# Performance work log

Measured on AMD Instinct MI355X. Metric: run time of the kernel, lower is better.

## Reference

```python
import jax, jax.numpy as jnp
import numpy as np

B, T, D = 32, 1024, 384
MAX_LEN = 8192

def setup_inputs() -> dict:
    key = jax.random.key(0)
    k1, k2 = jax.random.split(key)
    x = jax.random.normal(k1, (B, T, D), dtype=jnp.float32)
    duration = jax.random.randint(k2, (B, T), 0, 8, dtype=jnp.int32)
    return {"x": x, "duration": duration, "max_len": MAX_LEN}

def reference(x, duration, max_len):
    # x: [B, T, D] float, duration: [B, T] int, max_len: python int
    # Token t occupies output frames [cumsum[t-1], cumsum[t]).
    csum = jnp.cumsum(duration, axis=-1)            # [B, T]
    frames = jnp.arange(max_len, dtype=csum.dtype)  # [L]
    # For frame j, token index = # of cumsum entries <= j (searchsorted right).
    idx = jax.vmap(lambda c: jnp.searchsorted(c, frames, side='right'))(csum)  # [B, L]
    mel_len = csum[:, -1]                           # [B]
    valid = frames[None, :] < mel_len[:, None]      # [B, L]
    idx_c = jnp.clip(idx, 0, x.shape[1] - 1)
    out = jnp.take_along_axis(x, idx_c[:, :, None], axis=1)  # [B, L, D]
    out = jnp.where(valid[:, :, None], out, jnp.zeros((), dtype=x.dtype))
    return out, mel_len.astype(jnp.int32)
```

## Files before the change

kernel.cpp:

```cpp
#include <hip/hip_runtime.h>
#include <hip/hip_bf16.h>


#define LR_B 32
#define LR_T 1024
#define LR_D 384
#define LR_MAXLEN 8192
#define LR_D4 (LR_D / 4)
#define LR_N4 (LR_B * LR_MAXLEN * LR_D4)

__global__ __launch_bounds__(LR_T) void lr_scan_scatter(
    const int* __restrict__ dur,
    int* __restrict__ idx_ws,
    float* __restrict__ mel_out)
{
    const int b = blockIdx.x;
    const int t = threadIdx.x;
    __shared__ int csum[LR_T];

    csum[t] = dur[b * LR_T + t];
    __syncthreads();

    #pragma unroll
    for (int off = 1; off < LR_T; off <<= 1) {
        int v = csum[t];
        int add = (t >= off) ? csum[t - off] : 0;
        __syncthreads();
        csum[t] = v + add;
        __syncthreads();
    }

    const int total = csum[LR_T - 1];
    if (t == 0) mel_out[b] = (float)total;

    int end = csum[t];
    int start = (t == 0) ? 0 : csum[t - 1];
    int* row = idx_ws + b * LR_MAXLEN;
    for (int f = start; f < end; ++f) row[f] = t;

    for (int f = total + t; f < LR_MAXLEN; f += LR_T) row[f] = -1;
}

__global__ __launch_bounds__(256) void lr_gather(
    const float4* __restrict__ x,
    const int* __restrict__ idx_ws,
    float4* __restrict__ out)
{
    const int g = blockIdx.x * 256 + threadIdx.x;
    const int frame = g / LR_D4;
    const int e = g - frame * LR_D4;
    const int b = frame >> 13;
    const int idx = idx_ws[frame];

    float4 v = make_float4(0.f, 0.f, 0.f, 0.f);
    if (idx >= 0) {
        v = x[(b * LR_T + idx) * LR_D4 + e];
    }
    out[g] = v;
}

extern "C" void kernel_launch(void* const* d_in, const int* in_sizes, int n_in,
                              void* d_out, int out_size, void* d_ws, size_t ws_size,
                              hipStream_t stream) {
    const float* x   = (const float*)d_in[0];
    const int*   dur = (const int*)d_in[1];

    float* out0 = (float*)d_out;
    float* mel  = out0 + (size_t)LR_B * LR_MAXLEN * LR_D;
    int*   idx_ws = (int*)d_ws;

    lr_scan_scatter<<<LR_B, LR_T, 0, stream>>>(dur, idx_ws, mel);

    const int n_blocks = LR_N4 / 256;
    lr_gather<<<n_blocks, 256, 0, stream>>>(
        (const float4*)x, idx_ws, (float4*)out0);
}
```

Baseline: 443.8 us.

## Use wave-shuffle scan, precomputed source offsets, unrolled gather with nontemporal stores

The scan kernel replaces the shared-memory Hillis-Steele scan with a two-level wave shuffle scan, which cuts the number of block barriers. The scatter now writes precomputed element offsets into x, so the gather skips the batch and row index arithmetic. The gather kernel handles 8 float4 elements per thread with unrolling and uses nontemporal stores for the large output write, aiming to raise memory-level parallelism and avoid polluting the cache. This gives fewer blocks and more registers per thread.

```diff
diff --git a/kernel.cpp b/kernel.cpp
--- a/kernel.cpp
+++ b/kernel.cpp
@@ -8,55 +8,74 @@
 #define LR_MAXLEN 8192
 #define LR_D4 (LR_D / 4)
 #define LR_N4 (LR_B * LR_MAXLEN * LR_D4)
+#define LR_UNROLL 8
+
+typedef float fx4 __attribute__((ext_vector_type(4)));
 
 __global__ __launch_bounds__(LR_T) void lr_scan_scatter(
     const int* __restrict__ dur,
-    int* __restrict__ idx_ws,
+    int* __restrict__ src_ws,
     float* __restrict__ mel_out)
 {
     const int b = blockIdx.x;
     const int t = threadIdx.x;
-    __shared__ int csum[LR_T];
+    const int lane = t & 63;
+    const int wave = t >> 6;
 
-    csum[t] = dur[b * LR_T + t];
+    const int d = dur[b * LR_T + t];
+
+    int v = d;
+    #pragma unroll
+    for (int off = 1; off < 64; off <<= 1) {
+        int n = __shfl_up(v, off, 64);
+        if (lane >= off) v += n;
+    }
+
+    __shared__ int wsum[16];
+    __shared__ int woff[16];
+    if (lane == 63) wsum[wave] = v;
     __syncthreads();
 
-    #pragma unroll
-    for (int off = 1; off < LR_T; off <<= 1) {
-        int v = csum[t];
-        int add = (t >= off) ? csum[t - off] : 0;
-        __syncthreads();
-        csum[t] = v + add;
-        __syncthreads();
+    if (wave == 0 && lane < 16) {
+        int s = wsum[lane];
+        #pragma unroll
+        for (int off = 1; off < 16; off <<= 1) {
+            int n = __shfl_up(s, off, 64);
+            if (lane >= off) s += n;
+        }
+        woff[lane] = s;
     }
+    __syncthreads();
 
-    const int total = csum[LR_T - 1];
+    const int base  = (wave == 0) ? 0 : woff[wave - 1];
+    const int end   = base + v;
+    const int start = end - d;
+    const int total = woff[15];
+
     if (t == 0) mel_out[b] = (float)total;
 
-    int end = csum[t];
-    int start = (t == 0) ? 0 : csum[t - 1];
-    int* row = idx_ws + b * LR_MAXLEN;
-    for (int f = start; f < end; ++f) row[f] = t;
-
+    int* row = src_ws + b * LR_MAXLEN;
+    const int src_off = (b * LR_T + t) * LR_D4;
+    for (int f = start; f < end; ++f) row[f] = src_off;
     for (int f = total + t; f < LR_MAXLEN; f += LR_T) row[f] = -1;
 }
 
 __global__ __launch_bounds__(256) void lr_gather(
-    const float4* __restrict__ x,
-    const int* __restrict__ idx_ws,
-    float4* __restrict__ out)
+    const fx4* __restrict__ x,
+    const int* __restrict__ src_ws,
+    fx4* __restrict__ out)
 {
-    const int g = blockIdx.x * 256 + threadIdx.x;
-    const int frame = g / LR_D4;
-    const int e = g - frame * LR_D4;
-    const int b = frame >> 13;
-    const int idx = idx_ws[frame];
-
-    float4 v = make_float4(0.f, 0.f, 0.f, 0.f);
-    if (idx >= 0) {
-        v = x[(b * LR_T + idx) * LR_D4 + e];
+    const unsigned base = blockIdx.x * (256u * LR_UNROLL) + threadIdx.x;
+    #pragma unroll
+    for (int u = 0; u < LR_UNROLL; ++u) {
+        const unsigned g = base + u * 256u;
+        const unsigned frame = g / LR_D4;
+        const unsigned e = g - frame * LR_D4;
+        const int s = src_ws[frame];
+        fx4 v = (fx4)(0.f, 0.f, 0.f, 0.f);
+        if (s >= 0) v = x[(unsigned)s + e];
+        __builtin_nontemporal_store(v, out + g);
     }
-    out[g] = v;
 }
 
 extern "C" void kernel_launch(void* const* d_in, const int* in_sizes, int n_in,
@@ -67,11 +86,11 @@
 
     float* out0 = (float*)d_out;
     float* mel  = out0 + (size_t)LR_B * LR_MAXLEN * LR_D;
-    int*   idx_ws = (int*)d_ws;
+    int*   src_ws = (int*)d_ws;
 
-    lr_scan_scatter<<<LR_B, LR_T, 0, stream>>>(dur, idx_ws, mel);
+    lr_scan_scatter<<<LR_B, LR_T, 0, stream>>>(dur, src_ws, mel);
 
-    const int n_blocks = LR_N4 / 256;
+    const int n_blocks = LR_N4 / (256 * LR_UNROLL);
     lr_gather<<<n_blocks, 256, 0, stream>>>(
-        (const float4*)x, idx_ws, (float4*)out0);
+        (const fx4*)x, src_ws, (fx4*)out0);
 }
```

After: 437.6 us. About the same (-1.4%).
